# Performance work log

Measured on AMD Instinct MI355X. Metric: run time of the kernel, lower is better.

## Reference

```python
import jax, jax.numpy as jnp
import numpy as np
from jax import lax

B, T, C, H, W, SV = 1, 12, 10, 256, 256, 3
LAMBDA = 0.05
ITERS = 10


def _to_c(x):
    return lax.complex(x[..., 0], x[..., 1])


def _to_r(x):
    return jnp.stack([jnp.real(x), jnp.imag(x)], axis=-1)


def fft_2d_img(x):
    # torch: fftshift(ifft2(ifftshift(x)))  (backward-norm ifft, same as numpy/jax)
    ax = (-2, -1)
    return jnp.fft.fftshift(jnp.fft.ifft2(jnp.fft.ifftshift(x, axes=ax), axes=ax), axes=ax)


def ifft_2d_img(x):
    ax = (-2, -1)
    return jnp.fft.ifftshift(jnp.fft.fft2(jnp.fft.fftshift(x, axes=ax), axes=ax), axes=ax)


def setup_inputs() -> dict:
    key = jax.random.key(0)
    k0, k1, k2, k3, k4 = jax.random.split(key, 5)
    y = jax.random.normal(k0, (B, T, C, H, W, 2), jnp.float32)
    model_out = jax.random.normal(k1, (B, SV, H, W, 2), jnp.float32)
    sens = jax.random.normal(k2, (B, 1, C, H, W, 2), jnp.float32)
    time_basis = jax.random.normal(k3, (B, T, SV, 2), jnp.float32)
    mask = (jax.random.uniform(k4, (B, T, 1, H, W)) > 0.5).astype(jnp.float32)
    return dict(y=y, model_out=model_out, sens=sens, time_basis=time_basis, mask=mask)


def _adjoint(kspace, sens):
    # kspace: [b,t,c,h,w], sens: [b,1,c,h,w] -> [b,t,h,w]
    img = ifft_2d_img(kspace)
    return jnp.sum(jnp.conj(sens) * img, axis=2)


def _forward_model(data, sens, mask):
    # data: [b,t,h,w] -> masked k-space [b,t,c,h,w]
    coil = sens * data[:, :, None, :, :]
    return mask * fft_2d_img(coil)


def _system_R(x, sens, L, mask):
    # x: [b,sv,h,w]; L: [b,t,sv]
    b, sv, h, w = x.shape
    expanded = jnp.einsum('bts,bsp->btp', L, x.reshape(b, sv, h * w)).reshape(b, L.shape[1], h, w)
    masked_k = _forward_model(expanded, sens, mask)
    comb = _adjoint(masked_k, sens)  # [b,t,h,w]
    fin = jnp.einsum('bts,btp->bsp', jnp.conj(L), comb.reshape(b, L.shape[1], h * w))
    return fin.reshape(b, sv, h, w) + LAMBDA * x


def _cg_solve(A, b_vec):
    z = jnp.zeros_like(b_vec)
    r = b_vec
    p = r
    rs = jnp.vdot(r, r)

    def body(i, state):
        z, r, p, rs = state
        Ap = A(p)
        alpha = rs / jnp.vdot(p, Ap)
        z = z + alpha * p
        r = r - alpha * Ap
        rs_new = jnp.vdot(r, r)
        p = r + (rs_new / rs) * p
        return (z, r, p, rs_new)

    z, _, _, _ = lax.fori_loop(0, ITERS, body, (z, r, p, rs))
    return z


def reference(y, model_out, sens, time_basis, mask):
    yc = _to_c(y)            # [b,t,c,h,w] complex64
    sc = _to_c(sens)         # [b,1,c,h,w]
    mo = _to_c(model_out)    # [b,sv,h,w]
    L = _to_c(time_basis)    # [b,t,sv]
    b, t, c, h, w = yc.shape
    sv = L.shape[-1]

    ah_y = _adjoint(yc, sc)  # [b,t,h,w]
    b_vec = jnp.einsum('bts,btp->bsp', jnp.conj(L), ah_y.reshape(b, t, h * w)).reshape(b, sv, h, w)
    b_vec = b_vec + LAMBDA * mo

    A = lambda x: _system_R(x, sc, L, mask)
    z = _cg_solve(A, b_vec)  # [b,sv,h,w] complex
    return _to_r(z)          # [b,sv,h,w,2] float32
```

## Files before the change

kernel.cpp:

```cpp
#include <hip/hip_runtime.h>
#include <math.h>

#define HW 65536
#define NC 10
#define NT 12
#define LAMBDA_F 0.05f
#define PI_F 3.14159265358979323846f
#define SWZ(i) ((i) ^ ((i) >> 4))

__device__ __forceinline__ float2 cadd(float2 a, float2 b){ return make_float2(a.x+b.x, a.y+b.y); }
__device__ __forceinline__ float2 csub(float2 a, float2 b){ return make_float2(a.x-b.x, a.y-b.y); }
__device__ __forceinline__ float2 cmul(float2 a, float2 b){ return make_float2(a.x*b.x-a.y*b.y, a.x*b.y+a.y*b.x); }
__device__ __forceinline__ float2 cmulj(float2 a, float2 b){ return make_float2(a.x*b.x+a.y*b.y, a.x*b.y-a.y*b.x); }
__device__ __forceinline__ float2 cscale(float2 a, float s){ return make_float2(a.x*s, a.y*s); }

template<int SIGN>
__device__ __forceinline__ void radix4_nt(float2& a0, float2& a1, float2& a2, float2& a3){
  float2 t0=cadd(a0,a2), t1=csub(a0,a2), t2=cadd(a1,a3), t3=csub(a1,a3);
  float2 t3r;
  if constexpr (SIGN < 0) t3r = make_float2(t3.y, -t3.x); else t3r = make_float2(-t3.y, t3.x);
  a0=cadd(t0,t2); a1=cadd(t1,t3r); a2=csub(t0,t2); a3=csub(t1,t3r);
}

template<int SIGN>
__device__ __forceinline__ void radix4_tw(float2& a0, float2& a1, float2& a2, float2& a3, float2 w){
  if constexpr (SIGN > 0) w.y = -w.y;
  float2 w2 = cmul(w, w);
  float2 w3 = cmul(w, w2);
  a1 = cmul(a1, w); a2 = cmul(a2, w2); a3 = cmul(a3, w3);
  radix4_nt<SIGN>(a0, a1, a2, a3);
}

__device__ __forceinline__ float2 twf(int e){
  float s, c;
  __sincosf(-2.0f*PI_F*(float)e*(1.0f/256.0f), &s, &c);
  return make_float2(c, s);
}

template<int SIGN>
__device__ __forceinline__ void fft256(float2* b, int j,
                                       float2 wA, float2 wB, float2 wC,
                                       float2& x0, float2& x1, float2& x2, float2& x3){
  radix4_nt<SIGN>(x0,x1,x2,x3);
  b[SWZ(4*j)]=x0; b[SWZ(4*j+1)]=x1; b[SWZ(4*j+2)]=x2; b[SWZ(4*j+3)]=x3;
  x0=b[SWZ(j)]; x1=b[SWZ(j+64)]; x2=b[SWZ(j+128)]; x3=b[SWZ(j+192)];
  radix4_tw<SIGN>(x0,x1,x2,x3, wA);
  { int i=((j>>2)<<4)+(j&3); b[SWZ(i)]=x0; b[SWZ(i+4)]=x1; b[SWZ(i+8)]=x2; b[SWZ(i+12)]=x3; }
  x0=b[SWZ(j)]; x1=b[SWZ(j+64)]; x2=b[SWZ(j+128)]; x3=b[SWZ(j+192)];
  radix4_tw<SIGN>(x0,x1,x2,x3, wB);
  { int i=((j>>4)<<6)+(j&15); b[SWZ(i)]=x0; b[SWZ(i+16)]=x1; b[SWZ(i+32)]=x2; b[SWZ(i+48)]=x3; }
  x0=b[SWZ(j)]; x1=b[SWZ(j+64)]; x2=b[SWZ(j+128)]; x3=b[SWZ(j+192)];
  radix4_tw<SIGN>(x0,x1,x2,x3, wC);
}

__device__ __forceinline__ void cg_scalars(const float* __restrict__ scal, int it,
                                           float& a_re, float& a_im, float& beta){
  float rs = scal[0]; a_re = 0.f; a_im = 0.f; beta = 0.f;
  for (int k = 0; k < it; k++){
    float pr = scal[8+8*k+0], pi = scal[8+8*k+1];
    float rr_ = scal[8+8*k+2], ri_ = scal[8+8*k+3];
    float aa = scal[8+8*k+4];
    float den = pr*pr + pi*pi;
    a_re =  rs*pr/den;
    a_im = -rs*pi/den;
    float re_ = a_re*rr_ - a_im*ri_;
    float rs_next = rs - 2.0f*re_ + (a_re*a_re + a_im*a_im)*aa;
    beta = rs_next/rs;
    rs = rs_next;
  }
}

__global__ __launch_bounds__(256) void k_setup(const float* __restrict__ mask,
                                               const float2* __restrict__ Lt,
                                               const float2* __restrict__ y,
                                               float* __restrict__ W9,
                                               float2* __restrict__ bufB){
  int tid = threadIdx.x;
  int u = blockIdx.x;
  if (u < 256){
    int kx = u, ky = tid;
    int mx = (kx + 128) & 255, my = (ky + 128) & 255;
    float d0=0.f,d1=0.f,d2=0.f;
    float2 o01=make_float2(0,0), o02=make_float2(0,0), o12=make_float2(0,0);
    for (int t = 0; t < NT; t++){
      float m = mask[t*HW + my*256 + mx];
      float2 l0 = Lt[t*3+0], l1 = Lt[t*3+1], l2 = Lt[t*3+2];
      d0 += m*(l0.x*l0.x + l0.y*l0.y);
      d1 += m*(l1.x*l1.x + l1.y*l1.y);
      d2 += m*(l2.x*l2.x + l2.y*l2.y);
      o01 = cadd(o01, cscale(cmulj(l0,l1), m));
      o02 = cadd(o02, cscale(cmulj(l0,l2), m));
      o12 = cadd(o12, cscale(cmulj(l1,l2), m));
    }
    const float nrm = 1.0f/65536.0f;
    int idx = kx*256 + ky;
    W9[idx]      = d0*nrm;  W9[idx+HW]   = d1*nrm;  W9[idx+2*HW] = d2*nrm;
    W9[idx+3*HW] = o01.x*nrm; W9[idx+4*HW] = o01.y*nrm;
    W9[idx+5*HW] = o02.x*nrm; W9[idx+6*HW] = o02.y*nrm;
    W9[idx+7*HW] = o12.x*nrm; W9[idx+8*HW] = o12.y*nrm;
  } else {
    int idx = (u-256)*256 + tid;
    int c = idx >> 16, pix = idx & (HW-1);
    int xx = pix & 255, yy2 = pix >> 8;
    float sg = ((xx + yy2) & 1) ? -1.0f : 1.0f;
    float2 a0=make_float2(0,0), a1=make_float2(0,0), a2=make_float2(0,0);
    for (int t = 0; t < NT; t++){
      float2 yv = y[((size_t)(t*NC + c))*HW + pix];
      a0 = cadd(a0, cmulj(Lt[t*3+0], yv));
      a1 = cadd(a1, cmulj(Lt[t*3+1], yv));
      a2 = cadd(a2, cmulj(Lt[t*3+2], yv));
    }
    bufB[((size_t)(c*3+0))*HW + pix] = cscale(a0, sg);
    bufB[((size_t)(c*3+1))*HW + pix] = cscale(a1, sg);
    bufB[((size_t)(c*3+2))*HW + pix] = cscale(a2, sg);
  }
}

__global__ __launch_bounds__(512) void k_rows_plain(const float2* __restrict__ src,
                                                    float2* __restrict__ dst){
  __shared__ float2 tile[8][256];
  int tid = threadIdx.x, g = tid >> 6, j = tid & 63;
  float2 wA = twf((j&3)<<4), wB = twf((j&15)<<2), wC = twf(j);
  int pl = blockIdx.y, ri = blockIdx.x;
  int row = ri*8 + g;
  const float2* sr = src + (size_t)pl*HW + row*256;
  float2 x0=sr[j], x1=sr[j+64], x2=sr[j+128], x3=sr[j+192];
  fft256<-1>(tile[g], j, wA,wB,wC, x0,x1,x2,x3);
  tile[g][j]=x0; tile[g][j+64]=x1; tile[g][j+128]=x2; tile[g][j+192]=x3;
  __syncthreads();
  float2* dT = dst + (size_t)pl*HW;
  int yo2 = (tid&3)*2, kxo = tid>>2;
  #pragma unroll
  for (int kb = 0; kb < 2; kb++){
    int kx = kb*128 + kxo;
    float2 a = tile[yo2][kx], b = tile[yo2+1][kx];
    *(float4*)(dT + (size_t)kx*256 + ri*8 + yo2) = make_float4(a.x,a.y,b.x,b.y);
  }
}

__global__ __launch_bounds__(512) void k_cols_plain(const float2* __restrict__ src,
                                                    float2* __restrict__ dst){
  __shared__ float2 tile[8][256];
  int tid = threadIdx.x, g = tid >> 6, j = tid & 63;
  float2 wA = twf((j&3)<<4), wB = twf((j&15)<<2), wC = twf(j);
  int pl = blockIdx.y, kg = blockIdx.x;
  int kx = kg*8 + g;
  const float2* col = src + (size_t)pl*HW + (size_t)kx*256;
  float2 x0=col[j], x1=col[j+64], x2=col[j+128], x3=col[j+192];
  fft256<-1>(tile[g], j, wA,wB,wC, x0,x1,x2,x3);
  tile[g][j]=x0; tile[g][j+64]=x1; tile[g][j+128]=x2; tile[g][j+192]=x3;
  __syncthreads();
  float2* d = dst + (size_t)pl*HW;
  int kxo2 = (tid&3)*2, yy = tid>>2;
  #pragma unroll
  for (int yb = 0; yb < 2; yb++){
    int yc = yb*128 + yy;
    float2 a = tile[kxo2][yc], b = tile[kxo2+1][yc];
    *(float4*)(d + (size_t)yc*256 + kg*8 + kxo2) = make_float4(a.x,a.y,b.x,b.y);
  }
}

__global__ __launch_bounds__(256) void k_compute_b(const float2* __restrict__ A,
                                                   const float2* __restrict__ sens,
                                                   const float2* __restrict__ mo,
                                                   float2* __restrict__ p,
                                                   float2* __restrict__ r,
                                                   float2* __restrict__ z,
                                                   float* __restrict__ part){
  __shared__ float red[4];
  int idx = blockIdx.x*256 + threadIdx.x;
  int s = idx >> 16, pix = idx & (HW-1);
  int xx = pix & 255, yy = pix >> 8;
  float sg = ((xx + yy) & 1) ? -1.0f : 1.0f;
  float2 accv = make_float2(0,0);
  for (int c = 0; c < NC; c++)
    accv = cadd(accv, cmulj(sens[(size_t)c*HW + pix], A[((size_t)(c*3+s))*HW + pix]));
  float2 b = cadd(cscale(accv, sg), cscale(mo[idx], LAMBDA_F));
  p[idx] = b; r[idx] = b; z[idx] = make_float2(0,0);
  float partv = b.x*b.x + b.y*b.y;
  for (int off = 32; off; off >>= 1) partv += __shfl_down(partv, off);
  int j = threadIdx.x & 63, w = threadIdx.x >> 6;
  if (j == 0) red[w] = partv;
  __syncthreads();
  if (threadIdx.x == 0) part[5*1024 + blockIdx.x] = red[0]+red[1]+red[2]+red[3];
}

__global__ __launch_bounds__(512) void k_rows_op(const float2* __restrict__ rprev,
                                                 const float2* __restrict__ pprev,
                                                 const float2* __restrict__ Apb,
                                                 float2* __restrict__ pout,
                                                 float2* __restrict__ rout,
                                                 float2* __restrict__ z,
                                                 const float2* __restrict__ sens,
                                                 float2* __restrict__ dst,
                                                 const float* __restrict__ scal, int iter){
  __shared__ float2 tile[8][256];
  int tid = threadIdx.x, g = tid >> 6, j = tid & 63;
  float2 wA = twf((j&3)<<4), wB = twf((j&15)<<2), wC = twf(j);
  int pl = blockIdx.y, ri = blockIdx.x;
  int c = pl/3, sp = pl - 3*c;
  int row = ri*8 + g;
  int base = row*256;
  const float2* Sp = sens + (size_t)c*HW;
  float a_re=0.f, a_im=0.f, beta=0.f;
  if (iter > 0) cg_scalars(scal, iter, a_re, a_im, beta);
  size_t pb = (size_t)sp*HW + base;
  float2 pv[4];
  if (iter == 0){
    pv[0]=pprev[pb+j]; pv[1]=pprev[pb+j+64]; pv[2]=pprev[pb+j+128]; pv[3]=pprev[pb+j+192];
  } else {
    #pragma unroll
    for (int q = 0; q < 4; q++){
      int x = j + 64*q;
      float2 pe = pprev[pb+x], re_ = rprev[pb+x], ae = Apb[pb+x];
      float2 rnew = make_float2(re_.x - (a_re*ae.x - a_im*ae.y),
                                re_.y - (a_re*ae.y + a_im*ae.x));
      pv[q] = make_float2(rnew.x + beta*pe.x, rnew.y + beta*pe.y);
      if (c == 0){
        rout[pb+x] = rnew;
        pout[pb+x] = pv[q];
        float2 ze = z[pb+x];
        z[pb+x] = make_float2(ze.x + a_re*pe.x - a_im*pe.y,
                              ze.y + a_re*pe.y + a_im*pe.x);
      }
    }
  }
  float2 x0 = cmul(Sp[base+j],     pv[0]);
  float2 x1 = cmul(Sp[base+j+64],  pv[1]);
  float2 x2 = cmul(Sp[base+j+128], pv[2]);
  float2 x3 = cmul(Sp[base+j+192], pv[3]);
  fft256<1>(tile[g], j, wA,wB,wC, x0,x1,x2,x3);
  tile[g][j]=x0; tile[g][j+64]=x1; tile[g][j+128]=x2; tile[g][j+192]=x3;
  __syncthreads();
  float2* dT = dst + (size_t)pl*HW;
  int yo2 = (tid&3)*2, kxo = tid>>2;
  #pragma unroll
  for (int kb = 0; kb < 2; kb++){
    int kx = kb*128 + kxo;
    float2 a = tile[yo2][kx], b = tile[yo2+1][kx];
    *(float4*)(dT + (size_t)kx*256 + ri*8 + yo2) = make_float4(a.x,a.y,b.x,b.y);
  }
}

__global__ __launch_bounds__(384) void k_cols_W(const float2* __restrict__ src,
                                                float2* __restrict__ dst,
                                                const float* __restrict__ W9){
  __shared__ float2 tile[6][256];
  int tid = threadIdx.x, w = tid >> 6, j = tid & 63;
  float2 wA = twf((j&3)<<4), wB = twf((j&15)<<2), wC = twf(j);
  int kg = blockIdx.x, c = blockIdx.y;
  int s = w >> 1, kxl = w & 1;
  int kx = kg*2 + kxl;
  {
    const float2* col = src + ((size_t)(c*3+s))*HW + (size_t)kx*256;
    float2 x0=col[j], x1=col[j+64], x2=col[j+128], x3=col[j+192];
    fft256<1>(tile[w], j, wA,wB,wC, x0,x1,x2,x3);
    tile[w][j]=x0; tile[w][j+64]=x1; tile[w][j+128]=x2; tile[w][j+192]=x3;
  }
  __syncthreads();
  float2 U[4];
  #pragma unroll
  for (int q = 0; q < 4; q++){
    int k = j + 64*q;
    int wi = kx*256 + k;
    float2 v0 = tile[0*2+kxl][k], v1 = tile[1*2+kxl][k], v2 = tile[2*2+kxl][k];
    if (s == 0){
      float d0 = W9[wi];
      float2 o01 = make_float2(W9[wi+3*HW], W9[wi+4*HW]);
      float2 o02 = make_float2(W9[wi+5*HW], W9[wi+6*HW]);
      U[q] = cadd(cadd(cscale(v0,d0), cmul(o01,v1)), cmul(o02,v2));
    } else if (s == 1){
      float d1 = W9[wi+HW];
      float2 o01 = make_float2(W9[wi+3*HW], W9[wi+4*HW]);
      float2 o12 = make_float2(W9[wi+7*HW], W9[wi+8*HW]);
      U[q] = cadd(cadd(cmulj(o01,v0), cscale(v1,d1)), cmul(o12,v2));
    } else {
      float d2 = W9[wi+2*HW];
      float2 o02 = make_float2(W9[wi+5*HW], W9[wi+6*HW]);
      float2 o12 = make_float2(W9[wi+7*HW], W9[wi+8*HW]);
      U[q] = cadd(cadd(cmulj(o02,v0), cmulj(o12,v1)), cscale(v2,d2));
    }
  }
  __syncthreads();
  {
    float2 x0=U[0], x1=U[1], x2=U[2], x3=U[3];
    fft256<-1>(tile[w], j, wA,wB,wC, x0,x1,x2,x3);
    tile[w][j]=x0; tile[w][j+64]=x1; tile[w][j+128]=x2; tile[w][j+192]=x3;
  }
  __syncthreads();
  int s_out = tid >> 7, yy = tid & 127;
  #pragma unroll
  for (int yb = 0; yb < 2; yb++){
    int yc = yb*128 + yy;
    float2 a = tile[s_out*2+0][yc], b = tile[s_out*2+1][yc];
    float2* d = dst + ((size_t)(c*3+s_out))*HW;
    *(float4*)(d + (size_t)yc*256 + kg*2) = make_float4(a.x,a.y,b.x,b.y);
  }
}

__global__ __launch_bounds__(640) void k_rows_acc(const float2* __restrict__ Bp,
                                                  const float2* __restrict__ sens,
                                                  const float2* __restrict__ p,
                                                  const float2* __restrict__ r,
                                                  float2* __restrict__ Ap,
                                                  float* __restrict__ part){
  __shared__ float2 scratch[10][256];
  __shared__ float red5[4][5];
  int tid = threadIdx.x, w = tid >> 6, j = tid & 63;
  float2 wA = twf((j&3)<<4), wB = twf((j&15)<<2), wC = twf(j);
  int row = blockIdx.x, s = blockIdx.y;
  {
    int c = w;
    const float2* src = Bp + ((size_t)(c*3+s))*HW + row*256;
    float2 x0=src[j], x1=src[j+64], x2=src[j+128], x3=src[j+192];
    fft256<-1>(scratch[w], j, wA,wB,wC, x0,x1,x2,x3);
    const float2* Sc = sens + (size_t)c*HW + row*256;
    scratch[w][j]     = cmulj(Sc[j],     x0);
    scratch[w][j+64]  = cmulj(Sc[j+64],  x1);
    scratch[w][j+128] = cmulj(Sc[j+128], x2);
    scratch[w][j+192] = cmulj(Sc[j+192], x3);
  }
  __syncthreads();
  if (tid < 256){
    int k = tid;
    float2 a = make_float2(0,0);
    #pragma unroll
    for (int c = 0; c < NC; c++) a = cadd(a, scratch[c][k]);
    size_t ob = (size_t)s*HW + row*256 + k;
    float2 pv = p[ob];
    float2 ap = cadd(a, cscale(pv, LAMBDA_F));
    Ap[ob] = ap;
    float2 rv = r[ob];
    float s0 = pv.x*ap.x + pv.y*ap.y;
    float s1 = pv.x*ap.y - pv.y*ap.x;
    float s2 = rv.x*ap.x + rv.y*ap.y;
    float s3 = rv.x*ap.y - rv.y*ap.x;
    float s4 = ap.x*ap.x + ap.y*ap.y;
    for (int off = 32; off; off >>= 1){
      s0 += __shfl_down(s0, off); s1 += __shfl_down(s1, off);
      s2 += __shfl_down(s2, off); s3 += __shfl_down(s3, off);
      s4 += __shfl_down(s4, off);
    }
    if (j == 0){ red5[w][0]=s0; red5[w][1]=s1; red5[w][2]=s2; red5[w][3]=s3; red5[w][4]=s4; }
  }
  __syncthreads();
  if (tid == 0){
    int bflat = blockIdx.y*256 + blockIdx.x;
    #pragma unroll
    for (int q = 0; q < 5; q++)
      part[q*1024 + bflat] = red5[0][q]+red5[1][q]+red5[2][q]+red5[3][q];
  }
}

__global__ __launch_bounds__(256) void k_reduce(float* __restrict__ scal,
                                                const float* __restrict__ part, int iter){
  __shared__ float red[4];
  int tid = threadIdx.x, j = tid & 63, w = tid >> 6;
  for (int q = 0; q < 5; q++){
    float v = part[q*1024 + tid] + part[q*1024 + tid + 256] + part[q*1024 + tid + 512];
    for (int off = 32; off; off >>= 1) v += __shfl_down(v, off);
    if (j == 0) red[w] = v;
    __syncthreads();
    if (tid == 0) scal[8+8*iter+q] = red[0]+red[1]+red[2]+red[3];
    __syncthreads();
  }
  if (iter == 0){
    float v = part[5*1024 + tid] + part[5*1024 + tid + 256] + part[5*1024 + tid + 512];
    for (int off = 32; off; off >>= 1) v += __shfl_down(v, off);
    if (j == 0) red[w] = v;
    __syncthreads();
    if (tid == 0) scal[0] = red[0]+red[1]+red[2]+red[3];
  }
}

__global__ __launch_bounds__(256) void k_zfin(float2* __restrict__ z,
                                              const float2* __restrict__ p9,
                                              const float* __restrict__ scal){
  float a_re, a_im, beta;
  cg_scalars(scal, 10, a_re, a_im, beta);
  int idx = blockIdx.x*256 + threadIdx.x;
  float2 pe = p9[idx], ze = z[idx];
  z[idx] = make_float2(ze.x + a_re*pe.x - a_im*pe.y,
                       ze.y + a_re*pe.y + a_im*pe.x);
}

extern "C" void kernel_launch(void* const* d_in, const int* in_sizes, int n_in,
                              void* d_out, int out_size, void* d_ws, size_t ws_size,
                              hipStream_t stream){
  const float2* y    = (const float2*)d_in[0];
  const float2* mo   = (const float2*)d_in[1];
  const float2* sens = (const float2*)d_in[2];
  const float2* Lt   = (const float2*)d_in[3];
  const float*  mask = (const float*)d_in[4];

  float* w = (float*)d_ws;
  float*  scal = w;
  float*  part = w + 128;
  float*  W9   = w + 128 + 6144;
  float2* bufA = (float2*)(W9 + 9*HW);
  float2* bufB = bufA + (size_t)30*HW;
  float2* p0   = bufB + (size_t)30*HW;
  float2* p1   = p0 + (size_t)3*HW;
  float2* r0   = p1 + (size_t)3*HW;
  float2* r1   = r0 + (size_t)3*HW;
  float2* Ap   = r1 + (size_t)3*HW;
  float2* z    = (float2*)d_out;

  k_setup<<<2816, 256, 0, stream>>>(mask, Lt, y, W9, bufB);
  k_rows_plain<<<dim3(32, 30), 512, 0, stream>>>(bufB, bufA);
  k_cols_plain<<<dim3(32, 30), 512, 0, stream>>>(bufA, bufB);
  k_compute_b<<<768, 256, 0, stream>>>(bufB, sens, mo, p0, r0, z, part);

  for (int it = 0; it < 10; it++){
    float2* pprev = (it == 0) ? p0 : ((it & 1) ? p0 : p1);
    float2* rprev = (it == 0) ? r0 : ((it & 1) ? r0 : r1);
    float2* pw = (it & 1) ? p1 : p0;
    float2* rw = (it & 1) ? r1 : r0;
    k_rows_op<<<dim3(32, 30), 512, 0, stream>>>(rprev, pprev, Ap, pw, rw, z, sens, bufA, scal, it);
    k_cols_W<<<dim3(128, 10), 384, 0, stream>>>(bufA, bufB, W9);
    k_rows_acc<<<dim3(256, 3), 640, 0, stream>>>(bufB, sens, pw, rw, Ap, part);
    k_reduce<<<1, 256, 0, stream>>>(scal, part, it);
  }
  k_zfin<<<768, 256, 0, stream>>>(z, p1, scal);
}
```

Measured before the change: 475.6 us.

## Fuse CG reduction into row kernel and process two FFT rows per wavefront

Removes the single-block k_reduce launch per CG iteration: every block of k_rows_op (and k_zfin) now reduces the partial sums redundantly and derives the CG scalars itself, with one block persisting them to scal. Separately, each wavefront now performs two 256-point FFTs at once (fft256x2), halving thread counts in rows_op, cols_W and rows_acc to raise ILP and amortize twiddles. The redundant per-block reduction adds global reads of the partial buffer, and halved thread counts reduce occupancy; the partial buffer is zeroed in setup since 1024 slots are now summed.

```diff
diff --git a/kernel.cpp b/kernel.cpp
--- a/kernel.cpp
+++ b/kernel.cpp
@@ -53,13 +53,41 @@
   radix4_tw<SIGN>(x0,x1,x2,x3, wC);
 }
 
-__device__ __forceinline__ void cg_scalars(const float* __restrict__ scal, int it,
-                                           float& a_re, float& a_im, float& beta){
-  float rs = scal[0]; a_re = 0.f; a_im = 0.f; beta = 0.f;
+template<int SIGN>
+__device__ __forceinline__ void fft256x2(float2* bA, float2* bB, int j,
+    float2 wA, float2 wB, float2 wC,
+    float2& a0, float2& a1, float2& a2, float2& a3,
+    float2& b0, float2& b1, float2& b2, float2& b3){
+  radix4_nt<SIGN>(a0,a1,a2,a3); radix4_nt<SIGN>(b0,b1,b2,b3);
+  bA[SWZ(4*j)]=a0; bA[SWZ(4*j+1)]=a1; bA[SWZ(4*j+2)]=a2; bA[SWZ(4*j+3)]=a3;
+  bB[SWZ(4*j)]=b0; bB[SWZ(4*j+1)]=b1; bB[SWZ(4*j+2)]=b2; bB[SWZ(4*j+3)]=b3;
+  a0=bA[SWZ(j)]; a1=bA[SWZ(j+64)]; a2=bA[SWZ(j+128)]; a3=bA[SWZ(j+192)];
+  b0=bB[SWZ(j)]; b1=bB[SWZ(j+64)]; b2=bB[SWZ(j+128)]; b3=bB[SWZ(j+192)];
+  radix4_tw<SIGN>(a0,a1,a2,a3, wA); radix4_tw<SIGN>(b0,b1,b2,b3, wA);
+  { int i=((j>>2)<<4)+(j&3);
+    bA[SWZ(i)]=a0; bA[SWZ(i+4)]=a1; bA[SWZ(i+8)]=a2; bA[SWZ(i+12)]=a3;
+    bB[SWZ(i)]=b0; bB[SWZ(i+4)]=b1; bB[SWZ(i+8)]=b2; bB[SWZ(i+12)]=b3; }
+  a0=bA[SWZ(j)]; a1=bA[SWZ(j+64)]; a2=bA[SWZ(j+128)]; a3=bA[SWZ(j+192)];
+  b0=bB[SWZ(j)]; b1=bB[SWZ(j+64)]; b2=bB[SWZ(j+128)]; b3=bB[SWZ(j+192)];
+  radix4_tw<SIGN>(a0,a1,a2,a3, wB); radix4_tw<SIGN>(b0,b1,b2,b3, wB);
+  { int i=((j>>4)<<6)+(j&15);
+    bA[SWZ(i)]=a0; bA[SWZ(i+16)]=a1; bA[SWZ(i+32)]=a2; bA[SWZ(i+48)]=a3;
+    bB[SWZ(i)]=b0; bB[SWZ(i+16)]=b1; bB[SWZ(i+32)]=b2; bB[SWZ(i+48)]=b3; }
+  a0=bA[SWZ(j)]; a1=bA[SWZ(j+64)]; a2=bA[SWZ(j+128)]; a3=bA[SWZ(j+192)];
+  b0=bB[SWZ(j)]; b1=bB[SWZ(j+64)]; b2=bB[SWZ(j+128)]; b3=bB[SWZ(j+192)];
+  radix4_tw<SIGN>(a0,a1,a2,a3, wC); radix4_tw<SIGN>(b0,b1,b2,b3, wC);
+}
+
+__device__ __forceinline__ void cg_chain(const float* __restrict__ scal,
+                                         float f0, float f1, float f2, float f3, float f4,
+                                         float rs0, int it,
+                                         float& a_re, float& a_im, float& beta){
+  float rs = rs0; a_re = 0.f; a_im = 0.f; beta = 0.f;
   for (int k = 0; k < it; k++){
-    float pr = scal[8+8*k+0], pi = scal[8+8*k+1];
-    float rr_ = scal[8+8*k+2], ri_ = scal[8+8*k+3];
-    float aa = scal[8+8*k+4];
+    float pr, pi, rr_, ri_, aa;
+    if (k == it-1){ pr=f0; pi=f1; rr_=f2; ri_=f3; aa=f4; }
+    else { pr=scal[8+8*k+0]; pi=scal[8+8*k+1]; rr_=scal[8+8*k+2];
+           ri_=scal[8+8*k+3]; aa=scal[8+8*k+4]; }
     float den = pr*pr + pi*pi;
     a_re =  rs*pr/den;
     a_im = -rs*pi/den;
@@ -74,9 +102,15 @@
                                                const float2* __restrict__ Lt,
                                                const float2* __restrict__ y,
                                                float* __restrict__ W9,
-                                               float2* __restrict__ bufB){
+                                               float2* __restrict__ bufB,
+                                               float* __restrict__ scal,
+                                               float* __restrict__ part){
   int tid = threadIdx.x;
   int u = blockIdx.x;
+  if (u == 0){
+    if (tid < 128) scal[tid] = 0.0f;
+    for (int i = tid; i < 6144; i += 256) part[i] = 0.0f;
+  }
   if (u < 256){
     int kx = u, ky = tid;
     int mx = (kx + 128) & 255, my = (ky + 128) & 255;
@@ -185,7 +219,7 @@
   if (threadIdx.x == 0) part[5*1024 + blockIdx.x] = red[0]+red[1]+red[2]+red[3];
 }
 
-__global__ __launch_bounds__(512) void k_rows_op(const float2* __restrict__ rprev,
+__global__ __launch_bounds__(256) void k_rows_op(const float2* __restrict__ rprev,
                                                  const float2* __restrict__ pprev,
                                                  const float2* __restrict__ Apb,
                                                  float2* __restrict__ pout,
@@ -193,50 +227,96 @@
                                                  float2* __restrict__ z,
                                                  const float2* __restrict__ sens,
                                                  float2* __restrict__ dst,
-                                                 const float* __restrict__ scal, int iter){
+                                                 float* __restrict__ scal,
+                                                 const float* __restrict__ part,
+                                                 int iter){
   __shared__ float2 tile[8][256];
+  __shared__ float red6[4][6];
   int tid = threadIdx.x, g = tid >> 6, j = tid & 63;
   float2 wA = twf((j&3)<<4), wB = twf((j&15)<<2), wC = twf(j);
   int pl = blockIdx.y, ri = blockIdx.x;
   int c = pl/3, sp = pl - 3*c;
-  int row = ri*8 + g;
-  int base = row*256;
   const float2* Sp = sens + (size_t)c*HW;
+
   float a_re=0.f, a_im=0.f, beta=0.f;
-  if (iter > 0) cg_scalars(scal, iter, a_re, a_im, beta);
-  size_t pb = (size_t)sp*HW + base;
-  float2 pv[4];
+  if (iter > 0){
+    float v[6];
+    #pragma unroll
+    for (int q = 0; q < 6; q++){
+      float x = part[q*1024+tid] + part[q*1024+tid+256]
+              + part[q*1024+tid+512] + part[q*1024+tid+768];
+      for (int off = 32; off; off >>= 1) x += __shfl_down(x, off);
+      v[q] = x;
+    }
+    if (j == 0){
+      #pragma unroll
+      for (int q = 0; q < 6; q++) red6[g][q] = v[q];
+    }
+    __syncthreads();
+    float f0 = red6[0][0]+red6[1][0]+red6[2][0]+red6[3][0];
+    float f1 = red6[0][1]+red6[1][1]+red6[2][1]+red6[3][1];
+    float f2 = red6[0][2]+red6[1][2]+red6[2][2]+red6[3][2];
+    float f3 = red6[0][3]+red6[1][3]+red6[2][3]+red6[3][3];
+    float f4 = red6[0][4]+red6[1][4]+red6[2][4]+red6[3][4];
+    float rs0 = (iter == 1) ? (red6[0][5]+red6[1][5]+red6[2][5]+red6[3][5]) : scal[0];
+    cg_chain(scal, f0,f1,f2,f3,f4, rs0, iter, a_re, a_im, beta);
+    if (blockIdx.x == 0 && blockIdx.y == 0 && tid == 0){
+      scal[8+8*(iter-1)+0]=f0; scal[8+8*(iter-1)+1]=f1; scal[8+8*(iter-1)+2]=f2;
+      scal[8+8*(iter-1)+3]=f3; scal[8+8*(iter-1)+4]=f4;
+      if (iter == 1) scal[0] = rs0;
+    }
+  }
+
+  int row0 = ri*8 + g*2, row1 = row0 + 1;
+  int baseA = row0*256, baseB = row1*256;
+  size_t pbA = (size_t)sp*HW + baseA, pbB = (size_t)sp*HW + baseB;
+  float2 pvA[4], pvB[4];
   if (iter == 0){
-    pv[0]=pprev[pb+j]; pv[1]=pprev[pb+j+64]; pv[2]=pprev[pb+j+128]; pv[3]=pprev[pb+j+192];
+    #pragma unroll
+    for (int q = 0; q < 4; q++){
+      pvA[q] = pprev[pbA + j + 64*q];
+      pvB[q] = pprev[pbB + j + 64*q];
+    }
   } else {
     #pragma unroll
     for (int q = 0; q < 4; q++){
       int x = j + 64*q;
-      float2 pe = pprev[pb+x], re_ = rprev[pb+x], ae = Apb[pb+x];
-      float2 rnew = make_float2(re_.x - (a_re*ae.x - a_im*ae.y),
-                                re_.y - (a_re*ae.y + a_im*ae.x));
-      pv[q] = make_float2(rnew.x + beta*pe.x, rnew.y + beta*pe.y);
+      float2 peA = pprev[pbA+x], reA = rprev[pbA+x], aeA = Apb[pbA+x];
+      float2 peB = pprev[pbB+x], reB = rprev[pbB+x], aeB = Apb[pbB+x];
+      float2 rnA = make_float2(reA.x - (a_re*aeA.x - a_im*aeA.y),
+                               reA.y - (a_re*aeA.y + a_im*aeA.x));
+      float2 rnB = make_float2(reB.x - (a_re*aeB.x - a_im*aeB.y),
+                               reB.y - (a_re*aeB.y + a_im*aeB.x));
+      pvA[q] = make_float2(rnA.x + beta*peA.x, rnA.y + beta*peA.y);
+      pvB[q] = make_float2(rnB.x + beta*peB.x, rnB.y + beta*peB.y);
       if (c == 0){
-        rout[pb+x] = rnew;
-        pout[pb+x] = pv[q];
-        float2 ze = z[pb+x];
-        z[pb+x] = make_float2(ze.x + a_re*pe.x - a_im*pe.y,
-                              ze.y + a_re*pe.y + a_im*pe.x);
+        rout[pbA+x] = rnA;  rout[pbB+x] = rnB;
+        pout[pbA+x] = pvA[q]; pout[pbB+x] = pvB[q];
+        float2 zA = z[pbA+x], zB = z[pbB+x];
+        z[pbA+x] = make_float2(zA.x + a_re*peA.x - a_im*peA.y,
+                               zA.y + a_re*peA.y + a_im*peA.x);
+        z[pbB+x] = make_float2(zB.x + a_re*peB.x - a_im*peB.y,
+                               zB.y + a_re*peB.y + a_im*peB.x);
       }
     }
   }
-  float2 x0 = cmul(Sp[base+j],     pv[0]);
-  float2 x1 = cmul(Sp[base+j+64],  pv[1]);
-  float2 x2 = cmul(Sp[base+j+128], pv[2]);
-  float2 x3 = cmul(Sp[base+j+192], pv[3]);
-  fft256<1>(tile[g], j, wA,wB,wC, x0,x1,x2,x3);
-  tile[g][j]=x0; tile[g][j+64]=x1; tile[g][j+128]=x2; tile[g][j+192]=x3;
+  float2 xA0 = cmul(Sp[baseA+j],     pvA[0]);
+  float2 xA1 = cmul(Sp[baseA+j+64],  pvA[1]);
+  float2 xA2 = cmul(Sp[baseA+j+128], pvA[2]);
+  float2 xA3 = cmul(Sp[baseA+j+192], pvA[3]);
+  float2 xB0 = cmul(Sp[baseB+j],     pvB[0]);
+  float2 xB1 = cmul(Sp[baseB+j+64],  pvB[1]);
+  float2 xB2 = cmul(Sp[baseB+j+128], pvB[2]);
+  float2 xB3 = cmul(Sp[baseB+j+192], pvB[3]);
+  fft256x2<1>(tile[g*2], tile[g*2+1], j, wA,wB,wC, xA0,xA1,xA2,xA3, xB0,xB1,xB2,xB3);
+  tile[g*2][j]=xA0; tile[g*2][j+64]=xA1; tile[g*2][j+128]=xA2; tile[g*2][j+192]=xA3;
+  tile[g*2+1][j]=xB0; tile[g*2+1][j+64]=xB1; tile[g*2+1][j+128]=xB2; tile[g*2+1][j+192]=xB3;
   __syncthreads();
   float2* dT = dst + (size_t)pl*HW;
   int yo2 = (tid&3)*2, kxo = tid>>2;
   #pragma unroll
-  for (int kb = 0; kb < 2; kb++){
-    int kx = kb*128 + kxo;
+  for (int kb = 0; kb < 4; kb++){
+    int kx = kb*64 + kxo;
     float2 a = tile[yo2][kx], b = tile[yo2+1][kx];
     *(float4*)(dT + (size_t)kx*256 + ri*8 + yo2) = make_float4(a.x,a.y,b.x,b.y);
   }
@@ -245,60 +325,91 @@
 __global__ __launch_bounds__(384) void k_cols_W(const float2* __restrict__ src,
                                                 float2* __restrict__ dst,
                                                 const float* __restrict__ W9){
-  __shared__ float2 tile[6][256];
+  __shared__ float2 tile[12][256];
   int tid = threadIdx.x, w = tid >> 6, j = tid & 63;
   float2 wA = twf((j&3)<<4), wB = twf((j&15)<<2), wC = twf(j);
   int kg = blockIdx.x, c = blockIdx.y;
-  int s = w >> 1, kxl = w & 1;
-  int kx = kg*2 + kxl;
+  int s = w >> 1, kxp = w & 1;
+  int kxl0 = kxp*2, kxl1 = kxl0+1;
+  int kx0 = kg*4 + kxl0, kx1 = kg*4 + kxl1;
   {
-    const float2* col = src + ((size_t)(c*3+s))*HW + (size_t)kx*256;
-    float2 x0=col[j], x1=col[j+64], x2=col[j+128], x3=col[j+192];
-    fft256<1>(tile[w], j, wA,wB,wC, x0,x1,x2,x3);
-    tile[w][j]=x0; tile[w][j+64]=x1; tile[w][j+128]=x2; tile[w][j+192]=x3;
-  }
-  __syncthreads();
-  float2 U[4];
+    const float2* colA = src + ((size_t)(c*3+s))*HW + (size_t)kx0*256;
+    const float2* colB = src + ((size_t)(c*3+s))*HW + (size_t)kx1*256;
+    float2 a0=colA[j], a1=colA[j+64], a2=colA[j+128], a3=colA[j+192];
+    float2 b0=colB[j], b1=colB[j+64], b2=colB[j+128], b3=colB[j+192];
+    fft256x2<1>(tile[s*4+kxl0], tile[s*4+kxl1], j, wA,wB,wC, a0,a1,a2,a3, b0,b1,b2,b3);
+    tile[s*4+kxl0][j]=a0; tile[s*4+kxl0][j+64]=a1; tile[s*4+kxl0][j+128]=a2; tile[s*4+kxl0][j+192]=a3;
+    tile[s*4+kxl1][j]=b0; tile[s*4+kxl1][j+64]=b1; tile[s*4+kxl1][j+128]=b2; tile[s*4+kxl1][j+192]=b3;
+  }
+  __syncthreads();
+  float2 UA[4], UB[4];
   #pragma unroll
   for (int q = 0; q < 4; q++){
     int k = j + 64*q;
-    int wi = kx*256 + k;
-    float2 v0 = tile[0*2+kxl][k], v1 = tile[1*2+kxl][k], v2 = tile[2*2+kxl][k];
-    if (s == 0){
-      float d0 = W9[wi];
-      float2 o01 = make_float2(W9[wi+3*HW], W9[wi+4*HW]);
-      float2 o02 = make_float2(W9[wi+5*HW], W9[wi+6*HW]);
-      U[q] = cadd(cadd(cscale(v0,d0), cmul(o01,v1)), cmul(o02,v2));
-    } else if (s == 1){
-      float d1 = W9[wi+HW];
-      float2 o01 = make_float2(W9[wi+3*HW], W9[wi+4*HW]);
-      float2 o12 = make_float2(W9[wi+7*HW], W9[wi+8*HW]);
-      U[q] = cadd(cadd(cmulj(o01,v0), cscale(v1,d1)), cmul(o12,v2));
-    } else {
-      float d2 = W9[wi+2*HW];
-      float2 o02 = make_float2(W9[wi+5*HW], W9[wi+6*HW]);
-      float2 o12 = make_float2(W9[wi+7*HW], W9[wi+8*HW]);
-      U[q] = cadd(cadd(cmulj(o02,v0), cmulj(o12,v1)), cscale(v2,d2));
+    {
+      int wi = kx0*256 + k;
+      float2 v0 = tile[0+kxl0][k], v1 = tile[4+kxl0][k], v2 = tile[8+kxl0][k];
+      if (s == 0){
+        float d0 = W9[wi];
+        float2 o01 = make_float2(W9[wi+3*HW], W9[wi+4*HW]);
+        float2 o02 = make_float2(W9[wi+5*HW], W9[wi+6*HW]);
+        UA[q] = cadd(cadd(cscale(v0,d0), cmul(o01,v1)), cmul(o02,v2));
+      } else if (s == 1){
+        float d1 = W9[wi+HW];
+        float2 o01 = make_float2(W9[wi+3*HW], W9[wi+4*HW]);
+        float2 o12 = make_float2(W9[wi+7*HW], W9[wi+8*HW]);
+        UA[q] = cadd(cadd(cmulj(o01,v0), cscale(v1,d1)), cmul(o12,v2));
+      } else {
+        float d2 = W9[wi+2*HW];
+        float2 o02 = make_float2(W9[wi+5*HW], W9[wi+6*HW]);
+        float2 o12 = make_float2(W9[wi+7*HW], W9[wi+8*HW]);
+        UA[q] = cadd(cadd(cmulj(o02,v0), cmulj(o12,v1)), cscale(v2,d2));
+      }
+    }
+    {
+      int wi = kx1*256 + k;
+      float2 v0 = tile[0+kxl1][k], v1 = tile[4+kxl1][k], v2 = tile[8+kxl1][k];
+      if (s == 0){
+        float d0 = W9[wi];
+        float2 o01 = make_float2(W9[wi+3*HW], W9[wi+4*HW]);
+        float2 o02 = make_float2(W9[wi+5*HW], W9[wi+6*HW]);
+        UB[q] = cadd(cadd(cscale(v0,d0), cmul(o01,v1)), cmul(o02,v2));
+      } else if (s == 1){
+        float d1 = W9[wi+HW];
+        float2 o01 = make_float2(W9[wi+3*HW], W9[wi+4*HW]);
+        float2 o12 = make_float2(W9[wi+7*HW], W9[wi+8*HW]);
+        UB[q] = cadd(cadd(cmulj(o01,v0), cscale(v1,d1)), cmul(o12,v2));
+      } else {
+        float d2 = W9[wi+2*HW];
+        float2 o02 = make_float2(W9[wi+5*HW], W9[wi+6*HW]);
+        float2 o12 = make_float2(W9[wi+7*HW], W9[wi+8*HW]);
+        UB[q] = cadd(cadd(cmulj(o02,v0), cmulj(o12,v1)), cscale(v2,d2));
+      }
     }
   }
   __syncthreads();
   {
-    float2 x0=U[0], x1=U[1], x2=U[2], x3=U[3];
-    fft256<-1>(tile[w], j, wA,wB,wC, x0,x1,x2,x3);
-    tile[w][j]=x0; tile[w][j+64]=x1; tile[w][j+128]=x2; tile[w][j+192]=x3;
-  }
-  __syncthreads();
-  int s_out = tid >> 7, yy = tid & 127;
+    float2 a0=UA[0], a1=UA[1], a2=UA[2], a3=UA[3];
+    float2 b0=UB[0], b1=UB[1], b2=UB[2], b3=UB[3];
+    fft256x2<-1>(tile[s*4+kxl0], tile[s*4+kxl1], j, wA,wB,wC, a0,a1,a2,a3, b0,b1,b2,b3);
+    tile[s*4+kxl0][j]=a0; tile[s*4+kxl0][j+64]=a1; tile[s*4+kxl0][j+128]=a2; tile[s*4+kxl0][j+192]=a3;
+    tile[s*4+kxl1][j]=b0; tile[s*4+kxl1][j+64]=b1; tile[s*4+kxl1][j+128]=b2; tile[s*4+kxl1][j+192]=b3;
+  }
+  __syncthreads();
   #pragma unroll
-  for (int yb = 0; yb < 2; yb++){
-    int yc = yb*128 + yy;
-    float2 a = tile[s_out*2+0][yc], b = tile[s_out*2+1][yc];
+  for (int yb = 0; yb < 4; yb++){
+    int flat = yb*384 + tid;
+    int s_out = flat >> 9;
+    int rem = flat & 511;
+    int kxo2 = (rem >> 8) << 1;
+    int yc = rem & 255;
+    float2 a = tile[s_out*4+kxo2][yc], b = tile[s_out*4+kxo2+1][yc];
     float2* d = dst + ((size_t)(c*3+s_out))*HW;
-    *(float4*)(d + (size_t)yc*256 + kg*2) = make_float4(a.x,a.y,b.x,b.y);
-  }
-}
-
-__global__ __launch_bounds__(640) void k_rows_acc(const float2* __restrict__ Bp,
+    *(float4*)(d + (size_t)yc*256 + kg*4 + kxo2) = make_float4(a.x,a.y,b.x,b.y);
+  }
+}
+
+__global__ __launch_bounds__(320) void k_rows_acc(const float2* __restrict__ Bp,
                                                   const float2* __restrict__ sens,
                                                   const float2* __restrict__ p,
                                                   const float2* __restrict__ r,
@@ -310,15 +421,22 @@
   float2 wA = twf((j&3)<<4), wB = twf((j&15)<<2), wC = twf(j);
   int row = blockIdx.x, s = blockIdx.y;
   {
-    int c = w;
-    const float2* src = Bp + ((size_t)(c*3+s))*HW + row*256;
-    float2 x0=src[j], x1=src[j+64], x2=src[j+128], x3=src[j+192];
-    fft256<-1>(scratch[w], j, wA,wB,wC, x0,x1,x2,x3);
-    const float2* Sc = sens + (size_t)c*HW + row*256;
-    scratch[w][j]     = cmulj(Sc[j],     x0);
-    scratch[w][j+64]  = cmulj(Sc[j+64],  x1);
-    scratch[w][j+128] = cmulj(Sc[j+128], x2);
-    scratch[w][j+192] = cmulj(Sc[j+192], x3);
+    int c0 = 2*w, c1 = 2*w+1;
+    const float2* srcA = Bp + ((size_t)(c0*3+s))*HW + row*256;
+    const float2* srcB = Bp + ((size_t)(c1*3+s))*HW + row*256;
+    float2 a0=srcA[j], a1=srcA[j+64], a2=srcA[j+128], a3=srcA[j+192];
+    float2 b0=srcB[j], b1=srcB[j+64], b2=srcB[j+128], b3=srcB[j+192];
+    fft256x2<-1>(scratch[c0], scratch[c1], j, wA,wB,wC, a0,a1,a2,a3, b0,b1,b2,b3);
+    const float2* ScA = sens + (size_t)c0*HW + row*256;
+    const float2* ScB = sens + (size_t)c1*HW + row*256;
+    scratch[c0][j]     = cmulj(ScA[j],     a0);
+    scratch[c0][j+64]  = cmulj(ScA[j+64],  a1);
+    scratch[c0][j+128] = cmulj(ScA[j+128], a2);
+    scratch[c0][j+192] = cmulj(ScA[j+192], a3);
+    scratch[c1][j]     = cmulj(ScB[j],     b0);
+    scratch[c1][j+64]  = cmulj(ScB[j+64],  b1);
+    scratch[c1][j+128] = cmulj(ScB[j+128], b2);
+    scratch[c1][j+192] = cmulj(ScB[j+192], b3);
   }
   __syncthreads();
   if (tid < 256){
@@ -352,33 +470,33 @@
   }
 }
 
-__global__ __launch_bounds__(256) void k_reduce(float* __restrict__ scal,
-                                                const float* __restrict__ part, int iter){
-  __shared__ float red[4];
-  int tid = threadIdx.x, j = tid & 63, w = tid >> 6;
-  for (int q = 0; q < 5; q++){
-    float v = part[q*1024 + tid] + part[q*1024 + tid + 256] + part[q*1024 + tid + 512];
-    for (int off = 32; off; off >>= 1) v += __shfl_down(v, off);
-    if (j == 0) red[w] = v;
-    __syncthreads();
-    if (tid == 0) scal[8+8*iter+q] = red[0]+red[1]+red[2]+red[3];
-    __syncthreads();
-  }
-  if (iter == 0){
-    float v = part[5*1024 + tid] + part[5*1024 + tid + 256] + part[5*1024 + tid + 512];
-    for (int off = 32; off; off >>= 1) v += __shfl_down(v, off);
-    if (j == 0) red[w] = v;
-    __syncthreads();
-    if (tid == 0) scal[0] = red[0]+red[1]+red[2]+red[3];
-  }
-}
-
 __global__ __launch_bounds__(256) void k_zfin(float2* __restrict__ z,
                                               const float2* __restrict__ p9,
-                                              const float* __restrict__ scal){
+                                              const float* __restrict__ scal,
+                                              const float* __restrict__ part){
+  __shared__ float red5[4][5];
+  int tid = threadIdx.x, g = tid >> 6, j = tid & 63;
+  float v[5];
+  #pragma unroll
+  for (int q = 0; q < 5; q++){
+    float x = part[q*1024+tid] + part[q*1024+tid+256]
+            + part[q*1024+tid+512] + part[q*1024+tid+768];
+    for (int off = 32; off; off >>= 1) x += __shfl_down(x, off);
+    v[q] = x;
+  }
+  if (j == 0){
+    #pragma unroll
+    for (int q = 0; q < 5; q++) red5[g][q] = v[q];
+  }
+  __syncthreads();
+  float f0 = red5[0][0]+red5[1][0]+red5[2][0]+red5[3][0];
+  float f1 = red5[0][1]+red5[1][1]+red5[2][1]+red5[3][1];
+  float f2 = red5[0][2]+red5[1][2]+red5[2][2]+red5[3][2];
+  float f3 = red5[0][3]+red5[1][3]+red5[2][3]+red5[3][3];
+  float f4 = red5[0][4]+red5[1][4]+red5[2][4]+red5[3][4];
   float a_re, a_im, beta;
-  cg_scalars(scal, 10, a_re, a_im, beta);
-  int idx = blockIdx.x*256 + threadIdx.x;
+  cg_chain(scal, f0,f1,f2,f3,f4, scal[0], 10, a_re, a_im, beta);
+  int idx = blockIdx.x*256 + tid;
   float2 pe = p9[idx], ze = z[idx];
   z[idx] = make_float2(ze.x + a_re*pe.x - a_im*pe.y,
                        ze.y + a_re*pe.y + a_im*pe.x);
@@ -406,7 +524,7 @@
   float2* Ap   = r1 + (size_t)3*HW;
   float2* z    = (float2*)d_out;
 
-  k_setup<<<2816, 256, 0, stream>>>(mask, Lt, y, W9, bufB);
+  k_setup<<<2816, 256, 0, stream>>>(mask, Lt, y, W9, bufB, scal, part);
   k_rows_plain<<<dim3(32, 30), 512, 0, stream>>>(bufB, bufA);
   k_cols_plain<<<dim3(32, 30), 512, 0, stream>>>(bufA, bufB);
   k_compute_b<<<768, 256, 0, stream>>>(bufB, sens, mo, p0, r0, z, part);
@@ -416,10 +534,9 @@
     float2* rprev = (it == 0) ? r0 : ((it & 1) ? r0 : r1);
     float2* pw = (it & 1) ? p1 : p0;
     float2* rw = (it & 1) ? r1 : r0;
-    k_rows_op<<<dim3(32, 30), 512, 0, stream>>>(rprev, pprev, Ap, pw, rw, z, sens, bufA, scal, it);
-    k_cols_W<<<dim3(128, 10), 384, 0, stream>>>(bufA, bufB, W9);
-    k_rows_acc<<<dim3(256, 3), 640, 0, stream>>>(bufB, sens, pw, rw, Ap, part);
-    k_reduce<<<1, 256, 0, stream>>>(scal, part, it);
-  }
-  k_zfin<<<768, 256, 0, stream>>>(z, p1, scal);
-}
+    k_rows_op<<<dim3(32, 30), 256, 0, stream>>>(rprev, pprev, Ap, pw, rw, z, sens, bufA, scal, part, it);
+    k_cols_W<<<dim3(64, 10), 384, 0, stream>>>(bufA, bufB, W9);
+    k_rows_acc<<<dim3(256, 3), 320, 0, stream>>>(bufB, sens, pw, rw, Ap, part);
+  }
+  k_zfin<<<768, 256, 0, stream>>>(z, p1, scal, part);
+}
```

Measured after the change: 474.1 us. No clear change (-0.3%).
